# Optimization experiments

Measured on AMD Instinct MI355X. Metric: run time of the kernel, lower is better.

Reference implementation:

```python
import jax, jax.numpy as jnp
import numpy as np

S0, S1, S2 = 256, 256, 16
SZ = np.array([S0, S1, S2], dtype=np.float32)
B, C_IN, N_PTS, T_TOTAL = 8, 4, 200, 32
NUMEL = 10 * (((S0 - 6) // 2 - 4) // 2) * (((S1 - 6) // 2 - 4) // 2) * S2  # 576000


def _make_consts():
    ii, jj, kk = np.meshgrid(np.arange(S0), np.arange(S1), np.arange(S2), indexing='ij')
    grid_pts = np.stack([ii, jj, kk], -1).reshape(-1, 3).astype(np.float32)  # [L,3]
    # 2x2x1 tessellation centers
    tess = np.array([[(2 * r + 1) * S0 / 4.0, (2 * c + 1) * S1 / 4.0, S2 / 2.0]
                     for r in range(2) for c in range(2)], dtype=np.float32)
    d = np.linalg.norm(grid_pts[:, None, :] - tess[None, :, :], axis=-1)  # [L,4]
    e = np.exp(-d / 10.0)  # std=10
    dist = e / e.sum(1, keepdims=True)
    return jnp.asarray(grid_pts), jnp.asarray(dist)

GRID_PTS, DIST = _make_consts()


def grid_sample_3d(x, grid):
    # x: [B,C,D,H,W]; grid: [B,D,H,W,3] with grid[...,0]->W, [...,1]->H, [...,2]->D
    # trilinear, zero padding, align_corners=False (torch defaults)
    Bn, C, D, H, W = x.shape
    xl = jnp.moveaxis(x, 1, -1)  # [B,D,H,W,C]
    ix = ((grid[..., 0] + 1) * W - 1) * 0.5
    iy = ((grid[..., 1] + 1) * H - 1) * 0.5
    iz = ((grid[..., 2] + 1) * D - 1) * 0.5
    x0, y0, z0 = jnp.floor(ix), jnp.floor(iy), jnp.floor(iz)
    fx, fy, fz = ix - x0, iy - y0, iz - z0
    x0i, y0i, z0i = x0.astype(jnp.int32), y0.astype(jnp.int32), z0.astype(jnp.int32)
    b_idx = jnp.arange(Bn).reshape(-1, 1, 1, 1)
    out = jnp.zeros(grid.shape[:-1] + (C,), x.dtype)
    for dz in (0, 1):
        wz = fz if dz else 1.0 - fz
        zi = z0i + dz
        for dy in (0, 1):
            wy = fy if dy else 1.0 - fy
            yi = y0i + dy
            for dx in (0, 1):
                wx = fx if dx else 1.0 - fx
                xi = x0i + dx
                valid = (xi >= 0) & (xi < W) & (yi >= 0) & (yi < H) & (zi >= 0) & (zi < D)
                val = xl[b_idx, jnp.clip(zi, 0, D - 1), jnp.clip(yi, 0, H - 1), jnp.clip(xi, 0, W - 1)]
                w = (wz * wy * wx) * valid
                out = out + val * w[..., None]
    return jnp.moveaxis(out, -1, 1)


def _forward(x, conv1_w, conv1_b, conv2_w, conv2_b, fc1_w, fc1_b, fc2_w, fc2_b, P, centers, times):
    dn = ('NCDHW', 'OIDHW', 'NCDHW')
    pool = lambda z: jax.lax.reduce_window(z, -jnp.inf, jax.lax.max, (1, 1, 2, 2, 1), (1, 1, 2, 2, 1), 'VALID')
    # localization net: conv -> maxpool -> relu, twice
    z = jax.lax.conv_general_dilated(x, conv1_w, (1, 1, 1), 'VALID', dimension_numbers=dn) + conv1_b[None, :, None, None, None]
    z = jax.nn.relu(pool(z))
    z = jax.lax.conv_general_dilated(z, conv2_w, (1, 1, 1), 'VALID', dimension_numbers=dn) + conv2_b[None, :, None, None, None]
    z = jax.nn.relu(pool(z))
    z = z.reshape(z.shape[0], -1)  # [B, NUMEL]
    h = jax.nn.relu(z @ fc1_w.T + fc1_b)
    theta = jnp.tanh(h @ fc2_w.T + fc2_b).reshape(x.shape[0], 4, 6)  # [B, n_tess, 6]
    alpha = jnp.pi * theta[:, :, :3]
    trans = theta[:, :, 3:]
    # rigid_t: per-piece rotation + translation
    cos, sin = jnp.cos(alpha), jnp.sin(alpha)
    zz = jnp.zeros_like(cos[:, :, 0]); oo = jnp.ones_like(zz)
    Bn, Tn = trans.shape[:2]
    X = jnp.stack([cos[:, :, 0], -sin[:, :, 0], zz, sin[:, :, 0], cos[:, :, 0], zz, zz, zz, oo], 2).reshape(Bn, Tn, 3, 3)
    Y = jnp.stack([cos[:, :, 1], zz, sin[:, :, 1], zz, oo, zz, -sin[:, :, 1], zz, cos[:, :, 1]], 2).reshape(Bn, Tn, 3, 3)
    Z = jnp.stack([oo, zz, zz, zz, cos[:, :, 2], -sin[:, :, 2], zz, sin[:, :, 2], cos[:, :, 2]], 2).reshape(Bn, Tn, 3, 3)
    R = jnp.einsum('btmn,btnk,btks->btms', X, Y, Z)
    szv = jnp.asarray(SZ)
    center = szv / 2
    Tv = trans * szv[None, None, :] + jnp.einsum('m,btms->bts', center, jnp.eye(3, dtype=x.dtype)[None, None] - R)
    # piecewise flow: distance-weighted blend of per-piece rigid transforms
    flow = jnp.einsum('lk,btks,lt->bls', GRID_PTS, R, DIST) + jnp.einsum('bts,lt->bls', Tv, DIST)
    norm_flow = (2 * flow / szv - 1).reshape(Bn, S0, S1, S2, 3)
    grid_out = norm_flow[..., ::-1]  # flip to torch grid_sample (x,y,z) order
    X_t = grid_sample_3d(x, grid_out)
    # regularizer + moved points (gather flow at rounded positions)
    Pt = jnp.moveaxis(P[:, :, times], 2, 0)  # [B,N,3]
    def per_t(nf_t, P_t):
        idx = jnp.round(P_t).astype(jnp.int32)
        a = nf_t[idx[:, 0], idx[:, 1], idx[:, 2]]  # [N,3]
        return 2 * P_t - (0.5 + 0.5 * a) * (szv - 1)
    moved = jax.vmap(per_t)(norm_flow, Pt)  # [B,N,3]
    reg = jnp.sqrt(((moved - centers[None]) ** 2).sum(-1)).mean(-1)  # [B], cdist diag mean
    return X_t, grid_out, reg, moved


def setup_inputs() -> dict:
    key = jax.random.key(0)
    ks = jax.random.split(key, 12)
    sz1 = jnp.asarray(SZ) - 1
    return {
        'x': jax.random.uniform(ks[0], (B, C_IN, S0, S1, S2), jnp.float32),
        'times': jax.random.randint(ks[1], (B,), 0, T_TOTAL),
        'conv1_w': jax.random.normal(ks[2], (8, C_IN, 7, 7, 1), jnp.float32) * 0.05,
        'conv1_b': jax.random.normal(ks[3], (8,), jnp.float32) * 0.05,
        'conv2_w': jax.random.normal(ks[4], (10, 8, 5, 5, 1), jnp.float32) * 0.05,
        'conv2_b': jax.random.normal(ks[5], (10,), jnp.float32) * 0.05,
        'fc1_w': jax.random.normal(ks[6], (32, NUMEL), jnp.float32) * 0.002,
        'fc1_b': jax.random.normal(ks[7], (32,), jnp.float32) * 0.05,
        'fc2_w': jax.random.normal(ks[8], (24, 32), jnp.float32) * 0.05,
        'fc2_b': jax.random.normal(ks[9], (24,), jnp.float32) * 0.05,
        'P': jax.random.uniform(ks[10], (N_PTS, 3, T_TOTAL), jnp.float32) * sz1[None, :, None],
        'centers': jax.random.uniform(ks[11], (N_PTS, 3), jnp.float32) * sz1[None, :],
    }


def reference(x, times, conv1_w, conv1_b, conv2_w, conv2_b, fc1_w, fc1_b, fc2_w, fc2_b, P, centers):
    return _forward(x, conv1_w, conv1_b, conv2_w, conv2_b, fc1_w, fc1_b, fc2_w, fc2_b, P, centers, times)
```

## Files before the change

### kernel.cpp

```cpp
#include <hip/hip_runtime.h>
#include <math.h>

#define OUT_XT     0
#define OUT_GRID   33554432
#define OUT_REG    58720256
#define OUT_MOVED  58720264
#define FC1_K      576000

#define WS_BUF1    0
#define WS_BUF2    16000000
#define WS_PART    20608000
#define WS_RED     21184000
#define WS_RT      58720256

__global__ __launch_bounds__(256) void k_prep(const float* __restrict__ w1,
                                              const float* __restrict__ w2,
                                              float* __restrict__ wt1,
                                              float* __restrict__ wt2) {
  const int tid = threadIdx.x;
  for (int t = tid; t < 1568; t += 256) {
    int oc = t & 7, idx = t >> 3;
    int ic = idx / 49, dd = idx % 49;
    wt1[t] = w1[(oc * 4 + ic) * 49 + dd];
  }
  for (int t = tid; t < 2000; t += 256) {
    int oc = t % 10, idx = t / 10;
    int ic = idx / 25, dd = idx % 25;
    wt2[t] = w2[(oc * 8 + ic) * 25 + dd];
  }
}

#define C1_RS 22
#define C1_PS 322
__global__ __launch_bounds__(256) void k_conv1(const float* __restrict__ x,
                                               const float* __restrict__ wt1,
                                               const float* __restrict__ b1,
                                               float* __restrict__ buf1) {
  __shared__ float sIn[16 * C1_PS];
  const int tid = threadIdx.x;
  const int tx = blockIdx.x, ty = blockIdx.y, b = blockIdx.z;

  const int k = tid & 15;
  const int pix = tid >> 4;
  const int pyl = pix >> 2, pxl = pix & 3;
  const int row0 = ty * 8, col0 = tx * 16;

  int sq[5], srow[5], scol[5], sbase[5];
  bool sval[5];
#pragma unroll
  for (int it = 0; it < 5; ++it) {
    int t = tid + it * 256;
    int q = t & 3, pos = t >> 2;
    int coli = pos % 22, rowi = pos / 22;
    sq[it] = q;
    srow[it] = row0 + rowi;
    scol[it] = col0 + coli;
    sbase[it] = rowi * C1_RS + coli;
    sval[it] = (t < 1232) && (srow[it] < 256) && (scol[it] < 256);
  }

  const float4* __restrict__ x4 = reinterpret_cast<const float4*>(x);
  float4 st[5];

#define C1_LOAD(ICV) do {                                                    \
  _Pragma("unroll")                                                          \
  for (int it = 0; it < 5; ++it) {                                           \
    float4 v = make_float4(0.f, 0.f, 0.f, 0.f);                              \
    if (sval[it])                                                            \
      v = x4[(((b * 4 + (ICV)) * 256 + srow[it]) * 256 + scol[it]) * 4 + sq[it]]; \
    st[it] = v;                                                              \
  } } while (0)

#define C1_WRITE() do {                                                      \
  _Pragma("unroll")                                                          \
  for (int it = 0; it < 5; ++it) {                                           \
    if (it < 4 || tid < 208) {                                               \
      float* sp = &sIn[(4 * sq[it]) * C1_PS + sbase[it]];                    \
      sp[0 * C1_PS] = st[it].x;                                              \
      sp[1 * C1_PS] = st[it].y;                                              \
      sp[2 * C1_PS] = st[it].z;                                              \
      sp[3 * C1_PS] = st[it].w;                                              \
    }                                                                        \
  } } while (0)

  float acc[2][4][8];
#pragma unroll
  for (int a = 0; a < 2; ++a)
#pragma unroll
    for (int c = 0; c < 4; ++c)
#pragma unroll
      for (int oc = 0; oc < 8; ++oc) acc[a][c][oc] = 0.f;

  C1_LOAD(0);
  C1_WRITE();
  __syncthreads();

#pragma unroll 1
  for (int ic = 0; ic < 4; ++ic) {
    if (ic < 3) C1_LOAD(ic + 1);
#pragma unroll 1
    for (int dy = 0; dy < 7; ++dy) {
      float v[2][10];
#pragma unroll
      for (int a = 0; a < 2; ++a) {
        const int base = k * C1_PS + (2 * pyl + a + dy) * C1_RS + 4 * pxl;
#pragma unroll
        for (int j = 0; j < 5; ++j) {
          float2 f = *reinterpret_cast<const float2*>(&sIn[base + 2 * j]);
          v[a][2 * j] = f.x;
          v[a][2 * j + 1] = f.y;
        }
      }
      const float* __restrict__ wd = wt1 + ic * 392 + dy * 56;
#pragma unroll
      for (int dx = 0; dx < 7; ++dx) {
#pragma unroll
        for (int a = 0; a < 2; ++a)
#pragma unroll
          for (int c = 0; c < 4; ++c) {
            const float val = v[a][c + dx];
#pragma unroll
            for (int oc = 0; oc < 8; ++oc)
              acc[a][c][oc] = fmaf(val, wd[dx * 8 + oc], acc[a][c][oc]);
          }
      }
    }
    if (ic < 3) {
      __syncthreads();
      C1_WRITE();
      __syncthreads();
    }
  }
#undef C1_LOAD
#undef C1_WRITE

  const int py = ty * 4 + pyl;
  if (py < 125) {
#pragma unroll
    for (int cc = 0; cc < 2; ++cc) {
      const int px = tx * 8 + 2 * pxl + cc;
      if (px < 125) {
#pragma unroll
        for (int oc = 0; oc < 8; ++oc) {
          float m = fmaxf(fmaxf(acc[0][2 * cc][oc], acc[0][2 * cc + 1][oc]),
                          fmaxf(acc[1][2 * cc][oc], acc[1][2 * cc + 1][oc])) + b1[oc];
          buf1[(((b * 8 + oc) * 125 + py) * 125 + px) * 16 + k] = fmaxf(m, 0.f);
        }
      }
    }
  }
}

#define C2_RS 20
#define C2_PS 258
__global__ __launch_bounds__(256) void k_conv2(const float* __restrict__ in,
                                               const float* __restrict__ wt2,
                                               const float* __restrict__ b2,
                                               float* __restrict__ buf2) {
  __shared__ float sIn[16 * C2_PS];
  const int tid = threadIdx.x;
  const int tx = blockIdx.x, ty = blockIdx.y, b = blockIdx.z;

  const int k = tid & 15;
  const int pix = tid >> 4;
  const int pyl = pix >> 2, pxl = pix & 3;
  const int row0 = ty * 8, col0 = tx * 16;

  int sq[4], srow[4], scol[4], sbase[4];
  bool sval[4];
#pragma unroll
  for (int it = 0; it < 4; ++it) {
    int t = tid + it * 256;
    int q = t & 3, pos = t >> 2;
    int coli = pos % 20, rowi = pos / 20;
    sq[it] = q;
    srow[it] = row0 + rowi;
    scol[it] = col0 + coli;
    sbase[it] = rowi * C2_RS + coli;
    sval[it] = (t < 960) && (scol[it] < 125);
  }

  const float4* __restrict__ in4 = reinterpret_cast<const float4*>(in);
  float4 st[4];

#define C2_LOAD(ICV) do {                                                    \
  _Pragma("unroll")                                                          \
  for (int it = 0; it < 4; ++it) {                                           \
    float4 v = make_float4(0.f, 0.f, 0.f, 0.f);                              \
    if (sval[it])                                                            \
      v = in4[(((b * 8 + (ICV)) * 125 + srow[it]) * 125 + scol[it]) * 4 + sq[it]]; \
    st[it] = v;                                                              \
  } } while (0)

#define C2_WRITE() do {                                                      \
  _Pragma("unroll")                                                          \
  for (int it = 0; it < 4; ++it) {                                           \
    if (it < 3 || tid < 192) {                                               \
      float* sp = &sIn[(4 * sq[it]) * C2_PS + sbase[it]];                    \
      sp[0 * C2_PS] = st[it].x;                                              \
      sp[1 * C2_PS] = st[it].y;                                              \
      sp[2 * C2_PS] = st[it].z;                                              \
      sp[3 * C2_PS] = st[it].w;                                              \
    }                                                                        \
  } } while (0)

  float acc[2][4][10];
#pragma unroll
  for (int a = 0; a < 2; ++a)
#pragma unroll
    for (int c = 0; c < 4; ++c)
#pragma unroll
      for (int oc = 0; oc < 10; ++oc) acc[a][c][oc] = 0.f;

  C2_LOAD(0);
  C2_WRITE();
  __syncthreads();

#pragma unroll 1
  for (int ic = 0; ic < 8; ++ic) {
    if (ic < 7) C2_LOAD(ic + 1);
#pragma unroll 1
    for (int dy = 0; dy < 5; ++dy) {
      float v[2][8];
#pragma unroll
      for (int a = 0; a < 2; ++a) {
        const int base = k * C2_PS + (2 * pyl + a + dy) * C2_RS + 4 * pxl;
#pragma unroll
        for (int j = 0; j < 4; ++j) {
          float2 f = *reinterpret_cast<const float2*>(&sIn[base + 2 * j]);
          v[a][2 * j] = f.x;
          v[a][2 * j + 1] = f.y;
        }
      }
      const float* __restrict__ wd = wt2 + ic * 250 + dy * 50;
#pragma unroll
      for (int dx = 0; dx < 5; ++dx) {
#pragma unroll
        for (int a = 0; a < 2; ++a)
#pragma unroll
          for (int c = 0; c < 4; ++c) {
            const float val = v[a][c + dx];
#pragma unroll
            for (int oc = 0; oc < 10; ++oc)
              acc[a][c][oc] = fmaf(val, wd[dx * 10 + oc], acc[a][c][oc]);
          }
      }
    }
    if (ic < 7) {
      __syncthreads();
      C2_WRITE();
      __syncthreads();
    }
  }
#undef C2_LOAD
#undef C2_WRITE

  const int py = ty * 4 + pyl;
#pragma unroll
  for (int cc = 0; cc < 2; ++cc) {
    const int px = tx * 8 + 2 * pxl + cc;
    if (px < 60) {
#pragma unroll
      for (int oc = 0; oc < 10; ++oc) {
        float m = fmaxf(fmaxf(acc[0][2 * cc][oc], acc[0][2 * cc + 1][oc]),
                        fmaxf(acc[1][2 * cc][oc], acc[1][2 * cc + 1][oc])) + b2[oc];
        buf2[(((b * 10 + oc) * 60 + py) * 60 + px) * 16 + k] = fmaxf(m, 0.f);
      }
    }
  }
}

__global__ __launch_bounds__(256) void k_fc1(const float* __restrict__ z,
                                             const float* __restrict__ w,
                                             float* __restrict__ partial) {
  __shared__ float sW[32 * 260];
  __shared__ float sZ[8 * 256];
  const int bid = blockIdx.x, tid = threadIdx.x;
  const int k0 = bid * 256;

  for (int t = tid; t < 2048; t += 256) {
    int o = t >> 6, kq = t & 63;
    float4 v = *reinterpret_cast<const float4*>(w + o * FC1_K + k0 + 4 * kq);
    *reinterpret_cast<float4*>(&sW[o * 260 + 4 * kq]) = v;
  }
  for (int t = tid; t < 512; t += 256) {
    int b = t >> 6, kq = t & 63;
    *reinterpret_cast<float4*>(&sZ[b * 256 + 4 * kq]) =
        *reinterpret_cast<const float4*>(z + b * FC1_K + k0 + 4 * kq);
  }
  __syncthreads();

  const int b = tid >> 5, o = tid & 31;
  const float* __restrict__ zp = &sZ[b * 256];
  const float* __restrict__ wp = &sW[o * 260];
  float a0 = 0.f, a1 = 0.f, a2 = 0.f, a3 = 0.f;
  float a4 = 0.f, a5 = 0.f, a6 = 0.f, a7 = 0.f;
#pragma unroll
  for (int kk = 0; kk < 256; kk += 8) {
    float4 z0 = *reinterpret_cast<const float4*>(zp + kk);
    float4 w0 = *reinterpret_cast<const float4*>(wp + kk);
    float4 z1 = *reinterpret_cast<const float4*>(zp + kk + 4);
    float4 w1 = *reinterpret_cast<const float4*>(wp + kk + 4);
    a0 = fmaf(z0.x, w0.x, a0);
    a1 = fmaf(z0.y, w0.y, a1);
    a2 = fmaf(z0.z, w0.z, a2);
    a3 = fmaf(z0.w, w0.w, a3);
    a4 = fmaf(z1.x, w1.x, a4);
    a5 = fmaf(z1.y, w1.y, a5);
    a6 = fmaf(z1.z, w1.z, a6);
    a7 = fmaf(z1.w, w1.w, a7);
  }
  partial[bid * 256 + tid] = ((a0 + a1) + (a2 + a3)) + ((a4 + a5) + (a6 + a7));
}

__global__ __launch_bounds__(256) void k_red(const float* __restrict__ partial,
                                             float* __restrict__ red) {
  const int bl = blockIdx.x, tid = threadIdx.x;
  const float* __restrict__ p = partial + bl * 25 * 256 + tid;
  float s0 = 0.f, s1 = 0.f, s2 = 0.f, s3 = 0.f, s4 = 0.f;
#pragma unroll
  for (int i = 0; i < 25; i += 5) {
    s0 += p[i * 256];
    s1 += p[(i + 1) * 256];
    s2 += p[(i + 2) * 256];
    s3 += p[(i + 3) * 256];
    s4 += p[(i + 4) * 256];
  }
  red[bl * 256 + tid] = ((s0 + s1) + (s2 + s3)) + s4;
}

__global__ __launch_bounds__(256) void k_head(const float* __restrict__ red,
                                              const float* __restrict__ fc1_b,
                                              const float* __restrict__ fc2_w,
                                              const float* __restrict__ fc2_b,
                                              float* __restrict__ RT) {
  __shared__ float sH[256];
  __shared__ float sTh[8][24];
  const int tid = threadIdx.x;
  float s0 = 0.f, s1 = 0.f, s2 = 0.f, s3 = 0.f, s4 = 0.f;
#pragma unroll
  for (int c = 0; c < 90; c += 5) {
    s0 += red[c * 256 + tid];
    s1 += red[(c + 1) * 256 + tid];
    s2 += red[(c + 2) * 256 + tid];
    s3 += red[(c + 3) * 256 + tid];
    s4 += red[(c + 4) * 256 + tid];
  }
  const int o = tid & 31;
  sH[tid] = fmaxf(((s0 + s1) + (s2 + s3)) + s4 + fc1_b[o], 0.f);
  __syncthreads();
  if (tid < 192) {
    int b = tid / 24, o2 = tid % 24;
    float a = fc2_b[o2];
#pragma unroll
    for (int i = 0; i < 32; ++i) a = fmaf(sH[b * 32 + i], fc2_w[o2 * 32 + i], a);
    sTh[b][o2] = tanhf(a);
  }
  __syncthreads();
  if (tid < 32) {
    const int b = tid >> 2, t = tid & 3;
    const float PI = 3.14159265358979323846f;
    float a0 = PI * sTh[b][t * 6 + 0];
    float a1 = PI * sTh[b][t * 6 + 1];
    float a2 = PI * sTh[b][t * 6 + 2];
    float t0 = sTh[b][t * 6 + 3], t1 = sTh[b][t * 6 + 4], t2 = sTh[b][t * 6 + 5];
    float c0 = cosf(a0), s0v = sinf(a0);
    float c1 = cosf(a1), s1v = sinf(a1);
    float c2 = cosf(a2), s2v = sinf(a2);
    float R[3][3];
    R[0][0] = c0 * c1;
    R[0][1] = c0 * s1v * s2v - s0v * c2;
    R[0][2] = c0 * s1v * c2 + s0v * s2v;
    R[1][0] = s0v * c1;
    R[1][1] = s0v * s1v * s2v + c0 * c2;
    R[1][2] = s0v * s1v * c2 - c0 * s2v;
    R[2][0] = -s1v;
    R[2][1] = c1 * s2v;
    R[2][2] = c1 * c2;
    const float SZv[3] = {256.f, 256.f, 16.f};
    const float cen[3] = {128.f, 128.f, 8.f};
    const float tr[3] = {t0, t1, t2};
    float* rt = RT + (b * 4 + t) * 12;
#pragma unroll
    for (int kq = 0; kq < 3; ++kq)
#pragma unroll
      for (int s = 0; s < 3; ++s) rt[kq * 3 + s] = R[kq][s];
#pragma unroll
    for (int s = 0; s < 3; ++s)
      rt[9 + s] = tr[s] * SZv[s] + cen[s] - (128.f * R[0][s] + 128.f * R[1][s] + 8.f * R[2][s]);
  }
}

__global__ __launch_bounds__(256) void k_flow(const float* __restrict__ x,
                                              const float* __restrict__ RT,
                                              float* __restrict__ out) {
  const int raw = blockIdx.x;
  const int bid = (raw & 7) * 4096 + (raw >> 3);
  const int tid = threadIdx.x;
  const int b = bid >> 12;
  const int l = ((bid & 4095) << 8) | tid;
  const int i = l >> 12, j = (l >> 4) & 255, k = l & 15;
  const float fi = (float)i, fj = (float)j, fk = (float)k;
  const float* __restrict__ rt = RT + b * 48;

  const float txs[4] = {64.f, 64.f, 192.f, 192.f};
  const float tys[4] = {64.f, 192.f, 64.f, 192.f};
  float e[4], es = 0.f;
#pragma unroll
  for (int t = 0; t < 4; ++t) {
    float dx = fi - txs[t], dy = fj - tys[t], dz = fk - 8.f;
    float d = __builtin_amdgcn_sqrtf(fmaf(dx, dx, fmaf(dy, dy, dz * dz)));
    e[t] = __expf(-0.1f * d);
    es += e[t];
  }
  float inv = __builtin_amdgcn_rcpf(es);
  float f0 = 0.f, f1 = 0.f, f2 = 0.f;
#pragma unroll
  for (int t = 0; t < 4; ++t) {
    float wt = e[t] * inv;
    const float* r = rt + t * 12;
    f0 += wt * (fi * r[0] + fj * r[3] + fk * r[6] + r[9]);
    f1 += wt * (fi * r[1] + fj * r[4] + fk * r[7] + r[10]);
    f2 += wt * (fi * r[2] + fj * r[5] + fk * r[8] + r[11]);
  }
  float nf0 = f0 * (1.f / 128.f) - 1.f;
  float nf1 = f1 * (1.f / 128.f) - 1.f;
  float nf2 = f2 * 0.125f - 1.f;

  int gbase = OUT_GRID + ((b << 20) + l) * 3;
  __builtin_nontemporal_store(nf2, &out[gbase]);
  __builtin_nontemporal_store(nf1, &out[gbase + 1]);
  __builtin_nontemporal_store(nf0, &out[gbase + 2]);

  float ix = ((nf2 + 1.f) * 16.f - 1.f) * 0.5f;
  float iy = ((nf1 + 1.f) * 256.f - 1.f) * 0.5f;
  float iz = ((nf0 + 1.f) * 256.f - 1.f) * 0.5f;
  float xf = floorf(ix), yf = floorf(iy), zf = floorf(iz);
  float fx = ix - xf, fy = iy - yf, fz = iz - zf;
  int x0 = (int)xf, y0 = (int)yf, z0 = (int)zf;
  int x1 = x0 + 1, y1 = y0 + 1, z1 = z0 + 1;
  bool vx0 = ((unsigned)x0 < 16u), vx1 = ((unsigned)x1 < 16u);
  bool vy0 = ((unsigned)y0 < 256u), vy1 = ((unsigned)y1 < 256u);
  bool vz0 = ((unsigned)z0 < 256u), vz1 = ((unsigned)z1 < 256u);
  int cx0 = min(max(x0, 0), 15), cx1 = min(max(x1, 0), 15);
  int cy0 = min(max(y0, 0), 255), cy1 = min(max(y1, 0), 255);
  int cz0 = min(max(z0, 0), 255), cz1 = min(max(z1, 0), 255);
  float wx0 = 1.f - fx, wx1 = fx, wy0 = 1.f - fy, wy1 = fy, wz0 = 1.f - fz, wz1 = fz;

  const float wxa = vx0 ? wx0 : 0.f;
  const float wxb = vx1 ? wx1 : 0.f;
  const int base_x = min(cx0, 14);
  const int i0 = cx0 - base_x;
  const int i1 = cx1 - base_x;
  const float ca = (i0 ? 0.f : wxa) + (i1 ? 0.f : wxb);
  const float cb = (i0 ? wxa : 0.f) + (i1 ? wxb : 0.f);

  float W4[4];
  W4[0] = wz0 * wy0 * ((vz0 && vy0) ? 1.f : 0.f);
  W4[1] = wz0 * wy1 * ((vz0 && vy1) ? 1.f : 0.f);
  W4[2] = wz1 * wy0 * ((vz1 && vy0) ? 1.f : 0.f);
  W4[3] = wz1 * wy1 * ((vz1 && vy1) ? 1.f : 0.f);

  int ro[4];
  ro[0] = (cz0 << 12) + (cy0 << 4) + base_x;
  ro[1] = (cz0 << 12) + (cy1 << 4) + base_x;
  ro[2] = (cz1 << 12) + (cy0 << 4) + base_x;
  ro[3] = (cz1 << 12) + (cy1 << 4) + base_x;

  const float* __restrict__ xb0 = x + ((size_t)(b * 4) << 20);

  {
    float2 fa[4], fb[4];
#pragma unroll
    for (int q = 0; q < 4; ++q) __builtin_memcpy(&fa[q], xb0 + ro[q], 8);
#pragma unroll
    for (int q = 0; q < 4; ++q) __builtin_memcpy(&fb[q], xb0 + (1 << 20) + ro[q], 8);
    float s0 = 0.f, s1 = 0.f;
#pragma unroll
    for (int q = 0; q < 4; ++q) {
      s0 = fmaf(W4[q], fmaf(cb, fa[q].y, ca * fa[q].x), s0);
      s1 = fmaf(W4[q], fmaf(cb, fb[q].y, ca * fb[q].x), s1);
    }
    __builtin_nontemporal_store(s0, &out[OUT_XT + ((b * 4 + 0) << 20) + l]);
    __builtin_nontemporal_store(s1, &out[OUT_XT + ((b * 4 + 1) << 20) + l]);
  }
  {
    float2 fa[4], fb[4];
#pragma unroll
    for (int q = 0; q < 4; ++q) __builtin_memcpy(&fa[q], xb0 + (2 << 20) + ro[q], 8);
#pragma unroll
    for (int q = 0; q < 4; ++q) __builtin_memcpy(&fb[q], xb0 + (3 << 20) + ro[q], 8);
    float s0 = 0.f, s1 = 0.f;
#pragma unroll
    for (int q = 0; q < 4; ++q) {
      s0 = fmaf(W4[q], fmaf(cb, fa[q].y, ca * fa[q].x), s0);
      s1 = fmaf(W4[q], fmaf(cb, fb[q].y, ca * fb[q].x), s1);
    }
    __builtin_nontemporal_store(s0, &out[OUT_XT + ((b * 4 + 2) << 20) + l]);
    __builtin_nontemporal_store(s1, &out[OUT_XT + ((b * 4 + 3) << 20) + l]);
  }
}

__global__ __launch_bounds__(256) void k_tail(const float* __restrict__ P,
                                              const float* __restrict__ centers,
                                              const int* __restrict__ times,
                                              float* __restrict__ out) {
  const int b = blockIdx.x, tid = threadIdx.x;
  __shared__ float sred[256];
  float nrm = 0.f;
  if (tid < 200) {
    int tb = times[b];
    float p0 = P[tid * 96 + tb];
    float p1 = P[tid * 96 + 32 + tb];
    float p2 = P[tid * 96 + 64 + tb];
    int i0 = (int)rintf(p0), i1 = (int)rintf(p1), i2 = (int)rintf(p2);
    int lp = (i0 << 12) + (i1 << 4) + i2;
    int gb = OUT_GRID + ((b << 20) + lp) * 3;
    float a0 = out[gb + 2];
    float a1 = out[gb + 1];
    float a2 = out[gb + 0];
    float m0 = 2.f * p0 - (0.5f + 0.5f * a0) * 255.f;
    float m1 = 2.f * p1 - (0.5f + 0.5f * a1) * 255.f;
    float m2 = 2.f * p2 - (0.5f + 0.5f * a2) * 15.f;
    int mo = OUT_MOVED + (b * 200 + tid) * 3;
    out[mo] = m0;
    out[mo + 1] = m1;
    out[mo + 2] = m2;
    float d0 = m0 - centers[tid * 3];
    float d1 = m1 - centers[tid * 3 + 1];
    float d2 = m2 - centers[tid * 3 + 2];
    nrm = sqrtf(d0 * d0 + d1 * d1 + d2 * d2);
  }
  sred[tid] = nrm;
  __syncthreads();
  for (int s = 128; s > 0; s >>= 1) {
    if (tid < s) sred[tid] += sred[tid + s];
    __syncthreads();
  }
  if (tid == 0) out[OUT_REG + b] = sred[0] * 0.005f;
}

extern "C" void kernel_launch(void* const* d_in, const int* in_sizes, int n_in,
                              void* d_out, int out_size, void* d_ws, size_t ws_size,
                              hipStream_t stream) {
  const float* x = (const float*)d_in[0];
  const int* times = (const int*)d_in[1];
  const float* w1 = (const float*)d_in[2];
  const float* b1 = (const float*)d_in[3];
  const float* w2 = (const float*)d_in[4];
  const float* b2 = (const float*)d_in[5];
  const float* fw1 = (const float*)d_in[6];
  const float* fb1 = (const float*)d_in[7];
  const float* fw2 = (const float*)d_in[8];
  const float* fb2 = (const float*)d_in[9];
  const float* P = (const float*)d_in[10];
  const float* centers = (const float*)d_in[11];
  float* out = (float*)d_out;

  float* wt1 = (float*)d_ws;
  float* wt2 = wt1 + 1568;

  float* buf1 = out + WS_BUF1;
  float* buf2 = out + WS_BUF2;
  float* partial = out + WS_PART;
  float* red = out + WS_RED;
  float* RT = out + WS_RT;

  k_prep<<<1, 256, 0, stream>>>(w1, w2, wt1, wt2);
  k_conv1<<<dim3(16, 32, 8), 256, 0, stream>>>(x, wt1, b1, buf1);
  k_conv2<<<dim3(8, 15, 8), 256, 0, stream>>>(buf1, wt2, b2, buf2);
  k_fc1<<<2250, 256, 0, stream>>>(buf2, fw1, partial);
  k_red<<<90, 256, 0, stream>>>(partial, red);
  k_head<<<1, 256, 0, stream>>>(red, fb1, fw2, fb2, RT);
  k_flow<<<32768, 256, 0, stream>>>(x, RT, out);
  k_tail<<<8, 256, 0, stream>>>(P, centers, times, out);
}
```

Baseline: 454.7 us.

## Pack input-channel pairs into fp16 and use dot2 in conv kernels

Converts conv1 and conv2 to pack pairs of input channels into half2 values, both for the shared-memory input tile and for the pre-transposed weights. The inner loops then use the fp16 dot2 instruction with fp32 accumulation. This halves the FMA instruction count and the shared-memory footprint and reads per channel pair, and halves the number of channel-loop iterations and barriers. In exchange, inputs and weights lose precision from fp32 to fp16, which may exceed the reference tolerance, and each load stage now holds twice as many registers.

```diff
diff --git a/kernel.cpp b/kernel.cpp
--- a/kernel.cpp
+++ b/kernel.cpp
@@ -13,30 +13,52 @@
 #define WS_RED     21184000
 #define WS_RT      58720256
 
+typedef __fp16 half2v __attribute__((ext_vector_type(2)));
+
+__device__ __forceinline__ unsigned int packh2(float a, float b) {
+  half2v h = __builtin_amdgcn_cvt_pkrtz(a, b);
+  return __builtin_bit_cast(unsigned int, h);
+}
+
+__device__ __forceinline__ float dot2f(unsigned int a, unsigned int b, float c) {
+#if __has_builtin(__builtin_amdgcn_fdot2)
+  return __builtin_amdgcn_fdot2(__builtin_bit_cast(half2v, a),
+                                __builtin_bit_cast(half2v, b), c, false);
+#else
+  half2v ha = __builtin_bit_cast(half2v, a);
+  half2v hb = __builtin_bit_cast(half2v, b);
+  return fmaf((float)ha.y, (float)hb.y, fmaf((float)ha.x, (float)hb.x, c));
+#endif
+}
+
 __global__ __launch_bounds__(256) void k_prep(const float* __restrict__ w1,
                                               const float* __restrict__ w2,
-                                              float* __restrict__ wt1,
-                                              float* __restrict__ wt2) {
+                                              unsigned int* __restrict__ wt1p,
+                                              unsigned int* __restrict__ wt2p) {
   const int tid = threadIdx.x;
-  for (int t = tid; t < 1568; t += 256) {
+  for (int t = tid; t < 784; t += 256) {
     int oc = t & 7, idx = t >> 3;
-    int ic = idx / 49, dd = idx % 49;
-    wt1[t] = w1[(oc * 4 + ic) * 49 + dd];
-  }
-  for (int t = tid; t < 2000; t += 256) {
+    int icp = idx / 49, dd = idx % 49;
+    float lo = w1[(oc * 4 + 2 * icp) * 49 + dd];
+    float hi = w1[(oc * 4 + 2 * icp + 1) * 49 + dd];
+    wt1p[t] = packh2(lo, hi);
+  }
+  for (int t = tid; t < 1000; t += 256) {
     int oc = t % 10, idx = t / 10;
-    int ic = idx / 25, dd = idx % 25;
-    wt2[t] = w2[(oc * 8 + ic) * 25 + dd];
+    int icp = idx / 25, dd = idx % 25;
+    float lo = w2[(oc * 8 + 2 * icp) * 25 + dd];
+    float hi = w2[(oc * 8 + 2 * icp + 1) * 25 + dd];
+    wt2p[t] = packh2(lo, hi);
   }
 }
 
 #define C1_RS 22
 #define C1_PS 322
 __global__ __launch_bounds__(256) void k_conv1(const float* __restrict__ x,
-                                               const float* __restrict__ wt1,
+                                               const unsigned int* __restrict__ wt1p,
                                                const float* __restrict__ b1,
                                                float* __restrict__ buf1) {
-  __shared__ float sIn[16 * C1_PS];
+  __shared__ unsigned int sIn[16 * C1_PS];
   const int tid = threadIdx.x;
   const int tx = blockIdx.x, ty = blockIdx.y, b = blockIdx.z;
 
@@ -60,26 +82,30 @@
   }
 
   const float4* __restrict__ x4 = reinterpret_cast<const float4*>(x);
-  float4 st[5];
-
-#define C1_LOAD(ICV) do {                                                    \
+  float4 sta[5], stb[5];
+
+#define C1_LOAD(ICP) do {                                                    \
   _Pragma("unroll")                                                          \
   for (int it = 0; it < 5; ++it) {                                           \
-    float4 v = make_float4(0.f, 0.f, 0.f, 0.f);                              \
-    if (sval[it])                                                            \
-      v = x4[(((b * 4 + (ICV)) * 256 + srow[it]) * 256 + scol[it]) * 4 + sq[it]]; \
-    st[it] = v;                                                              \
+    float4 va = make_float4(0.f, 0.f, 0.f, 0.f);                             \
+    float4 vb = va;                                                          \
+    if (sval[it]) {                                                          \
+      va = x4[(((b * 4 + 2 * (ICP)) * 256 + srow[it]) * 256 + scol[it]) * 4 + sq[it]]; \
+      vb = x4[(((b * 4 + 2 * (ICP) + 1) * 256 + srow[it]) * 256 + scol[it]) * 4 + sq[it]]; \
+    }                                                                        \
+    sta[it] = va;                                                            \
+    stb[it] = vb;                                                            \
   } } while (0)
 
 #define C1_WRITE() do {                                                      \
   _Pragma("unroll")                                                          \
   for (int it = 0; it < 5; ++it) {                                           \
     if (it < 4 || tid < 208) {                                               \
-      float* sp = &sIn[(4 * sq[it]) * C1_PS + sbase[it]];                    \
-      sp[0 * C1_PS] = st[it].x;                                              \
-      sp[1 * C1_PS] = st[it].y;                                              \
-      sp[2 * C1_PS] = st[it].z;                                              \
-      sp[3 * C1_PS] = st[it].w;                                              \
+      unsigned int* sp = &sIn[(4 * sq[it]) * C1_PS + sbase[it]];             \
+      sp[0 * C1_PS] = packh2(sta[it].x, stb[it].x);                          \
+      sp[1 * C1_PS] = packh2(sta[it].y, stb[it].y);                          \
+      sp[2 * C1_PS] = packh2(sta[it].z, stb[it].z);                          \
+      sp[3 * C1_PS] = packh2(sta[it].w, stb[it].w);                          \
     }                                                                        \
   } } while (0)
 
@@ -96,36 +122,36 @@
   __syncthreads();
 
 #pragma unroll 1
-  for (int ic = 0; ic < 4; ++ic) {
-    if (ic < 3) C1_LOAD(ic + 1);
+  for (int icp = 0; icp < 2; ++icp) {
+    if (icp == 0) C1_LOAD(1);
 #pragma unroll 1
     for (int dy = 0; dy < 7; ++dy) {
-      float v[2][10];
+      unsigned int v2[2][10];
 #pragma unroll
       for (int a = 0; a < 2; ++a) {
         const int base = k * C1_PS + (2 * pyl + a + dy) * C1_RS + 4 * pxl;
 #pragma unroll
         for (int j = 0; j < 5; ++j) {
-          float2 f = *reinterpret_cast<const float2*>(&sIn[base + 2 * j]);
-          v[a][2 * j] = f.x;
-          v[a][2 * j + 1] = f.y;
+          uint2 f = *reinterpret_cast<const uint2*>(&sIn[base + 2 * j]);
+          v2[a][2 * j] = f.x;
+          v2[a][2 * j + 1] = f.y;
         }
       }
-      const float* __restrict__ wd = wt1 + ic * 392 + dy * 56;
+      const unsigned int* __restrict__ wd = wt1p + (icp * 49 + dy * 7) * 8;
 #pragma unroll
       for (int dx = 0; dx < 7; ++dx) {
 #pragma unroll
         for (int a = 0; a < 2; ++a)
 #pragma unroll
           for (int c = 0; c < 4; ++c) {
-            const float val = v[a][c + dx];
+            const unsigned int val = v2[a][c + dx];
 #pragma unroll
             for (int oc = 0; oc < 8; ++oc)
-              acc[a][c][oc] = fmaf(val, wd[dx * 8 + oc], acc[a][c][oc]);
+              acc[a][c][oc] = dot2f(val, wd[dx * 8 + oc], acc[a][c][oc]);
           }
       }
     }
-    if (ic < 3) {
+    if (icp == 0) {
       __syncthreads();
       C1_WRITE();
       __syncthreads();
@@ -154,10 +180,10 @@
 #define C2_RS 20
 #define C2_PS 258
 __global__ __launch_bounds__(256) void k_conv2(const float* __restrict__ in,
-                                               const float* __restrict__ wt2,
+                                               const unsigned int* __restrict__ wt2p,
                                                const float* __restrict__ b2,
                                                float* __restrict__ buf2) {
-  __shared__ float sIn[16 * C2_PS];
+  __shared__ unsigned int sIn[16 * C2_PS];
   const int tid = threadIdx.x;
   const int tx = blockIdx.x, ty = blockIdx.y, b = blockIdx.z;
 
@@ -181,26 +207,30 @@
   }
 
   const float4* __restrict__ in4 = reinterpret_cast<const float4*>(in);
-  float4 st[4];
-
-#define C2_LOAD(ICV) do {                                                    \
+  float4 sta[4], stb[4];
+
+#define C2_LOAD(ICP) do {                                                    \
   _Pragma("unroll")                                                          \
   for (int it = 0; it < 4; ++it) {                                           \
-    float4 v = make_float4(0.f, 0.f, 0.f, 0.f);                              \
-    if (sval[it])                                                            \
-      v = in4[(((b * 8 + (ICV)) * 125 + srow[it]) * 125 + scol[it]) * 4 + sq[it]]; \
-    st[it] = v;                                                              \
+    float4 va = make_float4(0.f, 0.f, 0.f, 0.f);                             \
+    float4 vb = va;                                                          \
+    if (sval[it]) {                                                          \
+      va = in4[(((b * 8 + 2 * (ICP)) * 125 + srow[it]) * 125 + scol[it]) * 4 + sq[it]]; \
+      vb = in4[(((b * 8 + 2 * (ICP) + 1) * 125 + srow[it]) * 125 + scol[it]) * 4 + sq[it]]; \
+    }                                                                        \
+    sta[it] = va;                                                            \
+    stb[it] = vb;                                                            \
   } } while (0)
 
 #define C2_WRITE() do {                                                      \
   _Pragma("unroll")                                                          \
   for (int it = 0; it < 4; ++it) {                                           \
     if (it < 3 || tid < 192) {                                               \
-      float* sp = &sIn[(4 * sq[it]) * C2_PS + sbase[it]];                    \
-      sp[0 * C2_PS] = st[it].x;                                              \
-      sp[1 * C2_PS] = st[it].y;                                              \
-      sp[2 * C2_PS] = st[it].z;                                              \
-      sp[3 * C2_PS] = st[it].w;                                              \
+      unsigned int* sp = &sIn[(4 * sq[it]) * C2_PS + sbase[it]];             \
+      sp[0 * C2_PS] = packh2(sta[it].x, stb[it].x);                          \
+      sp[1 * C2_PS] = packh2(sta[it].y, stb[it].y);                          \
+      sp[2 * C2_PS] = packh2(sta[it].z, stb[it].z);                          \
+      sp[3 * C2_PS] = packh2(sta[it].w, stb[it].w);                          \
     }                                                                        \
   } } while (0)
 
@@ -217,36 +247,36 @@
   __syncthreads();
 
 #pragma unroll 1
-  for (int ic = 0; ic < 8; ++ic) {
-    if (ic < 7) C2_LOAD(ic + 1);
+  for (int icp = 0; icp < 4; ++icp) {
+    if (icp < 3) C2_LOAD(icp + 1);
 #pragma unroll 1
     for (int dy = 0; dy < 5; ++dy) {
-      float v[2][8];
+      unsigned int v2[2][8];
 #pragma unroll
       for (int a = 0; a < 2; ++a) {
         const int base = k * C2_PS + (2 * pyl + a + dy) * C2_RS + 4 * pxl;
 #pragma unroll
         for (int j = 0; j < 4; ++j) {
-          float2 f = *reinterpret_cast<const float2*>(&sIn[base + 2 * j]);
-          v[a][2 * j] = f.x;
-          v[a][2 * j + 1] = f.y;
+          uint2 f = *reinterpret_cast<const uint2*>(&sIn[base + 2 * j]);
+          v2[a][2 * j] = f.x;
+          v2[a][2 * j + 1] = f.y;
         }
       }
-      const float* __restrict__ wd = wt2 + ic * 250 + dy * 50;
+      const unsigned int* __restrict__ wd = wt2p + (icp * 25 + dy * 5) * 10;
 #pragma unroll
       for (int dx = 0; dx < 5; ++dx) {
 #pragma unroll
         for (int a = 0; a < 2; ++a)
 #pragma unroll
           for (int c = 0; c < 4; ++c) {
-            const float val = v[a][c + dx];
+            const unsigned int val = v2[a][c + dx];
 #pragma unroll
             for (int oc = 0; oc < 10; ++oc)
-              acc[a][c][oc] = fmaf(val, wd[dx * 10 + oc], acc[a][c][oc]);
+              acc[a][c][oc] = dot2f(val, wd[dx * 10 + oc], acc[a][c][oc]);
           }
       }
     }
-    if (ic < 7) {
+    if (icp < 3) {
       __syncthreads();
       C2_WRITE();
       __syncthreads();
@@ -557,8 +587,8 @@
   const float* centers = (const float*)d_in[11];
   float* out = (float*)d_out;
 
-  float* wt1 = (float*)d_ws;
-  float* wt2 = wt1 + 1568;
+  unsigned int* wt1p = (unsigned int*)d_ws;
+  unsigned int* wt2p = wt1p + 784;
 
   float* buf1 = out + WS_BUF1;
   float* buf2 = out + WS_BUF2;
@@ -566,9 +596,9 @@
   float* red = out + WS_RED;
   float* RT = out + WS_RT;
 
-  k_prep<<<1, 256, 0, stream>>>(w1, w2, wt1, wt2);
-  k_conv1<<<dim3(16, 32, 8), 256, 0, stream>>>(x, wt1, b1, buf1);
-  k_conv2<<<dim3(8, 15, 8), 256, 0, stream>>>(buf1, wt2, b2, buf2);
+  k_prep<<<1, 256, 0, stream>>>(w1, w2, wt1p, wt2p);
+  k_conv1<<<dim3(16, 32, 8), 256, 0, stream>>>(x, wt1p, b1, buf1);
+  k_conv2<<<dim3(8, 15, 8), 256, 0, stream>>>(buf1, wt2p, b2, buf2);
   k_fc1<<<2250, 256, 0, stream>>>(buf2, fw1, partial);
   k_red<<<90, 256, 0, stream>>>(partial, red);
   k_head<<<1, 256, 0, stream>>>(red, fb1, fw2, fb2, RT);
```

Result: faster. 429.1 us (-5.6%).
